# Kernel optimization log

Measured on AMD Instinct MI355X. Metric: run time of the kernel, lower is better.

Reference implementation:

```python
import jax, jax.numpy as jnp
import numpy as np

D_MODEL = 1024
N_HEADS = 16
D_FF = 4096
EPS = 1e-5


def setup_inputs() -> dict:
    key = jax.random.key(0)
    ks = jax.random.split(key, 16)
    s = 0.02
    d, f = D_MODEL, D_FF
    return {
        "x": jax.random.normal(ks[0], (4, 2048, d), dtype=jnp.float32),
        "WQ": jax.random.normal(ks[1], (d, d), dtype=jnp.float32) * s,
        "bQ": jnp.zeros((d,), dtype=jnp.float32),
        "WK": jax.random.normal(ks[2], (d, d), dtype=jnp.float32) * s,
        "bK": jnp.zeros((d,), dtype=jnp.float32),
        "WV": jax.random.normal(ks[3], (d, d), dtype=jnp.float32) * s,
        "bV": jnp.zeros((d,), dtype=jnp.float32),
        "WO": jax.random.normal(ks[4], (d, d), dtype=jnp.float32) * s,
        "bO": jnp.zeros((d,), dtype=jnp.float32),
        "W1": jax.random.normal(ks[5], (f, d), dtype=jnp.float32) * s,
        "b1": jnp.zeros((f,), dtype=jnp.float32),
        "W2": jax.random.normal(ks[6], (d, f), dtype=jnp.float32) * s,
        "b2": jnp.zeros((d,), dtype=jnp.float32),
        "g1": jnp.ones((d,), dtype=jnp.float32),
        "be1": jnp.zeros((d,), dtype=jnp.float32),
        "g2": jnp.ones((d,), dtype=jnp.float32),
        "be2": jnp.zeros((d,), dtype=jnp.float32),
    }


def _layernorm(x, g, b):
    mu = jnp.mean(x, axis=-1, keepdims=True)
    var = jnp.mean(jnp.square(x - mu), axis=-1, keepdims=True)
    return (x - mu) * jax.lax.rsqrt(var + EPS) * g + b


def reference(x, WQ, bQ, WK, bK, WV, bV, WO, bO, W1, b1, W2, b2, g1, be1, g2, be2):
    B, T, D = x.shape
    H, dk = N_HEADS, D // N_HEADS
    # projections (torch Linear: x @ W.T + b), reshape to [B,H,T,dk]
    q = (x @ WQ.T + bQ).reshape(B, T, H, dk).transpose(0, 2, 1, 3)
    k = (x @ WK.T + bK).reshape(B, T, H, dk).transpose(0, 2, 1, 3)
    v = (x @ WV.T + bV).reshape(B, T, H, dk).transpose(0, 2, 1, 3)
    scores = jnp.einsum("bhqd,bhkd->bhqk", q, k) / jnp.sqrt(jnp.float32(dk))
    causal = jnp.tril(jnp.ones((T, T), dtype=bool))
    scores = jnp.where(causal[None, None], scores, jnp.float32(-jnp.inf))
    attn = jax.nn.softmax(scores, axis=-1)
    out = jnp.einsum("bhqk,bhkd->bhqd", attn, v)
    out = out.transpose(0, 2, 1, 3).reshape(B, T, D)
    attn_out = out @ WO.T + bO
    x = _layernorm(x + attn_out, g1, be1)
    ff = jax.nn.relu(x @ W1.T + b1) @ W2.T + b2
    return _layernorm(x + ff, g2, be2)
```

## Files before the change

### kernel.cpp

```cpp
#include <hip/hip_runtime.h>

typedef unsigned short u16;
typedef unsigned int u32;
typedef __bf16 bf16x8 __attribute__((ext_vector_type(8)));
typedef float f32x4 __attribute__((ext_vector_type(4)));

union U16x8 { uint4 u4; u16 us[8]; };

__device__ __forceinline__ u16 f2bf(float f) {
  u32 u = __builtin_bit_cast(u32, f);
  u = (u + 0x7fffu + ((u >> 16) & 1u)) >> 16;
  return (u16)u;
}
__device__ __forceinline__ float bf2f(u16 h) {
  return __builtin_bit_cast(float, ((u32)h) << 16);
}

__device__ __forceinline__ void gll16(const u16* g, u16* l) {
  __builtin_amdgcn_global_load_lds((const __attribute__((address_space(1))) void*)g,
                                   (__attribute__((address_space(3))) void*)l, 16, 0, 0);
}

__global__ __launch_bounds__(256) void cvt_all(const float* __restrict__ x,
                                               const float* __restrict__ WQ,
                                               const float* __restrict__ WK,
                                               const float* __restrict__ WV,
                                               const float* __restrict__ WO,
                                               const float* __restrict__ W1,
                                               const float* __restrict__ W2,
                                               u16* __restrict__ xb,
                                               u16* __restrict__ wqkvb,
                                               u16* __restrict__ wob,
                                               u16* __restrict__ w1b,
                                               u16* __restrict__ w2b) {
  const int S = 1 << 20;
  int i = (blockIdx.x * 256 + threadIdx.x) * 4;
  const float* src;
  u16* dst;
  if (i < 8 * S) { src = x + i; dst = xb + i; }
  else {
    int j = i - 8 * S;
    if (j < 3 * S)      { src = (j < S) ? WQ + j : (j < 2 * S) ? WK + (j - S) : WV + (j - 2 * S);
                          dst = wqkvb + j; }
    else if (j < 4 * S) { src = WO + (j - 3 * S); dst = wob + (j - 3 * S); }
    else if (j < 8 * S) { src = W1 + (j - 4 * S); dst = w1b + (j - 4 * S); }
    else                { src = W2 + (j - 8 * S); dst = w2b + (j - 8 * S); }
  }
  float4 v = *(const float4*)src;
  uint2 o;
  o.x = (u32)f2bf(v.x) | ((u32)f2bf(v.y) << 16);
  o.y = (u32)f2bf(v.z) | ((u32)f2bf(v.w) << 16);
  *(uint2*)dst = o;
}

template <int RELU, int OUT_BF16, int QKV, int SPLIT, int NBN>
__global__ __launch_bounds__(256) void gemm_bt(const u16* __restrict__ A,
                                               const u16* __restrict__ W,
                                               const float* __restrict__ bias0,
                                               void* __restrict__ C0,
                                               int M, int N, int K,
                                               const float* __restrict__ bias1,
                                               void* __restrict__ C1,
                                               const float* __restrict__ bias2,
                                               void* __restrict__ C2) {
  constexpr int NBNC = (NBN > 0) ? NBN : 1;
  __shared__ alignas(16) u16 sA[128 * 64];
  __shared__ alignas(16) u16 sB[128 * 64];
  const int tid = threadIdx.x;
  int bn, bm, koff = 0, KL = K, kz = 0;
  if (SPLIT) {
    const int id = blockIdx.x;
    const int within = id >> 3;
    const int G = (id & 7) + 8 * (within >> 3);
    bn = (within & 7) * 128;
    bm = (G & 63) * 128;
    kz = G >> 6;
    KL = K >> 1;
    koff = kz * KL;
  } else if (NBN > 0) {
    const int id = blockIdx.x;
    const int xcd = id & 7;
    const int r = id >> 3;
    bn = (r % NBNC) * 128;
    bm = ((r / NBNC) * 8 + xcd) * 128;
  } else {
    bn = blockIdx.x * 128;
    bm = blockIdx.y * 128;
  }
  const int lane = tid & 63, wave = tid >> 6;
  const int wm = (wave >> 1) * 64, wn = (wave & 1) * 64;
  const int lr = lane & 15, quad = lane >> 4;
  f32x4 acc[4][4] = {};

  const int srow8 = lane >> 3;
  const int sc = ((lane & 7) ^ srow8) * 8;
  const u16* Ap = A + (size_t)(bm + wave * 32 + srow8) * K + koff + sc;
  const u16* Wp = W + (size_t)(bn + wave * 32 + srow8) * K + koff + sc;
  u16* sAb = sA + wave * 32 * 64;
  u16* sBb = sB + wave * 32 * 64;
  const size_t rK8 = (size_t)8 * K;
  const int fsw = lr & 7;

  for (int kt = 0; kt < KL; kt += 64) {
    __syncthreads();
    #pragma unroll
    for (int j = 0; j < 4; j++) {
      gll16(Ap + kt + j * rK8, sAb + j * 8 * 64);
      gll16(Wp + kt + j * rK8, sBb + j * 8 * 64);
    }
    __syncthreads();
    #pragma unroll
    for (int sl = 0; sl < 2; sl++) {
      bf16x8 af[4], bfr[4];
      #pragma unroll
      for (int mi = 0; mi < 4; mi++)
        af[mi] = *(const bf16x8*)(sA + (wm + mi * 16 + lr) * 64 + ((((sl << 2) | quad) ^ fsw) * 8));
      #pragma unroll
      for (int ni = 0; ni < 4; ni++)
        bfr[ni] = *(const bf16x8*)(sB + (wn + ni * 16 + lr) * 64 + ((((sl << 2) | quad) ^ fsw) * 8));
      #pragma unroll
      for (int mi = 0; mi < 4; mi++)
        #pragma unroll
        for (int ni = 0; ni < 4; ni++)
          acc[mi][ni] = __builtin_amdgcn_mfma_f32_16x16x32_bf16(af[mi], bfr[ni], acc[mi][ni], 0, 0, 0);
    }
  }

  const float* bp = bias0;
  void* outp = C0;
  float scale = 1.0f;
  int cb = bn, Nout = N;
  int seg = 0;
  if (QKV) {
    Nout = 1024;
    seg = bn >> 10;
    cb = bn - (seg << 10);
    if (seg == 0) scale = 0.125f * 1.44269504089f;
    else if (seg == 1) { bp = bias1; outp = C1; }
    else { bp = bias2; outp = C2; }
  }
  if (SPLIT && kz) outp = C1;

  if (QKV && seg == 2) {
    #pragma unroll
    for (int ni = 0; ni < 4; ni++) {
      const int col = cb + wn + ni * 16 + lr;
      const int hh = col >> 6, dl = col & 63;
      const float bv = bp[col];
      #pragma unroll
      for (int mi = 0; mi < 4; mi++) {
        const int row0 = bm + wm + mi * 16 + quad * 4;
        const int bb = row0 >> 11, tt = row0 & 2047;
        u16 pk[4];
        #pragma unroll
        for (int rg = 0; rg < 4; rg++) pk[rg] = f2bf(acc[mi][ni][rg] + bv);
        uint2 val;
        val.x = (u32)pk[0] | ((u32)pk[1] << 16);
        val.y = (u32)pk[2] | ((u32)pk[3] << 16);
        *(uint2*)(((u16*)outp) + ((size_t)((bb * 16 + hh) * 64 + dl)) * 2048 + tt) = val;
      }
    }
    return;
  }

  #pragma unroll
  for (int ni = 0; ni < 4; ni++) {
    const int col = cb + wn + ni * 16 + lr;
    const float bv = (SPLIT && kz) ? 0.0f : bp[col];
    #pragma unroll
    for (int mi = 0; mi < 4; mi++) {
      #pragma unroll
      for (int rg = 0; rg < 4; rg++) {
        int row = bm + wm + mi * 16 + quad * 4 + rg;
        float v = (acc[mi][ni][rg] + bv) * scale;
        if (RELU) v = fmaxf(v, 0.0f);
        if (OUT_BF16) ((u16*)outp)[(size_t)row * Nout + col] = f2bf(v);
        else          ((float*)outp)[(size_t)row * Nout + col] = v;
      }
    }
  }
}

constexpr int ALD = 72;

__global__ __launch_bounds__(256) void attn_mfma(const u16* __restrict__ qb,
                                                 const u16* __restrict__ kb,
                                                 const u16* __restrict__ vt,
                                                 u16* __restrict__ ctxb, int T) {
  __shared__ alignas(16) u16 sK[64 * 64];
  __shared__ alignas(16) u16 sVt[64 * 64];
  __shared__ alignas(16) u16 sP[4 * 2 * 16 * ALD];
  const int tid = threadIdx.x;
  const int i = blockIdx.x;
  const int g = (i & 7) | (((i >> 7) & 7) << 3);
  const int p = (i >> 3) & 15;
  const int h = g >> 2, b = g & 3;
  const size_t base = ((size_t)(b * T)) * 1024 + h * 64;
  const size_t vbase = ((size_t)((b * 16 + h) * 64)) * T;
  const int lane = tid & 63, wave = tid >> 6;
  const int lr = lane & 15, quad = lane >> 4;
  u16* sPA = sP + (wave * 2) * 16 * ALD;
  u16* sPB = sPA + 16 * ALD;

  const int srow = lane >> 3;
  const int sch = ((lane & 7) ^ srow) * 8;
  const int fsw = lr & 7;

  const int qtA = 31 - p, qtB = p;
  const int q0A = qtA * 64 + wave * 16, q0B = qtB * 64 + wave * 16;
  bf16x8 qfA[2], qfB[2];
  #pragma unroll
  for (int sl = 0; sl < 2; sl++) {
    uint4 uA = *(const uint4*)(qb + base + (size_t)(q0A + lr) * 1024 + sl * 32 + quad * 8);
    qfA[sl] = __builtin_bit_cast(bf16x8, uA);
    uint4 uB = *(const uint4*)(qb + base + (size_t)(q0B + lr) * 1024 + sl * 32 + quad * 8);
    qfB[sl] = __builtin_bit_cast(bf16x8, uB);
  }
  f32x4 oA[4] = {}, oB[4] = {};
  float smA[4] = {0, 0, 0, 0}, smB[4] = {0, 0, 0, 0};

  for (int kt = 0; kt <= qtA; kt++) {
    const bool doB = (kt <= qtB);
    __syncthreads();
    #pragma unroll
    for (int j = 0; j < 2; j++) {
      const int rowbase = (wave * 2 + j) * 8;
      const int r = rowbase + srow;
      gll16(kb + base + (size_t)(kt * 64 + r) * 1024 + sch, sK + rowbase * 64);
      gll16(vt + vbase + (size_t)r * T + (size_t)(kt * 64) + sch, sVt + rowbase * 64);
    }
    __syncthreads();

    f32x4 sa[4] = {}, sb[4] = {};
    #pragma unroll
    for (int sl = 0; sl < 2; sl++) {
      bf16x8 kf[4];
      #pragma unroll
      for (int nt = 0; nt < 4; nt++)
        kf[nt] = *(const bf16x8*)(sK + (nt * 16 + lr) * 64 + ((((sl << 2) | quad) ^ fsw) * 8));
      #pragma unroll
      for (int nt = 0; nt < 4; nt++)
        sa[nt] = __builtin_amdgcn_mfma_f32_16x16x32_bf16(kf[nt], qfA[sl], sa[nt], 0, 0, 0);
      if (doB) {
        #pragma unroll
        for (int nt = 0; nt < 4; nt++)
          sb[nt] = __builtin_amdgcn_mfma_f32_16x16x32_bf16(kf[nt], qfB[sl], sb[nt], 0, 0, 0);
      }
    }

    const int qloc = wave * 16 + lr;
    if (kt == qtA) {
      #pragma unroll
      for (int nt = 0; nt < 4; nt++)
        #pragma unroll
        for (int rg = 0; rg < 4; rg++)
          if (nt * 16 + quad * 4 + rg > qloc) sa[nt][rg] = -1e30f;
    }
    if (doB && kt == qtB) {
      #pragma unroll
      for (int nt = 0; nt < 4; nt++)
        #pragma unroll
        for (int rg = 0; rg < 4; rg++)
          if (nt * 16 + quad * 4 + rg > qloc) sb[nt][rg] = -1e30f;
    }

    #pragma unroll
    for (int nt = 0; nt < 4; nt++) {
      float e0 = __builtin_amdgcn_exp2f(sa[nt][0]);
      float e1 = __builtin_amdgcn_exp2f(sa[nt][1]);
      float e2 = __builtin_amdgcn_exp2f(sa[nt][2]);
      float e3 = __builtin_amdgcn_exp2f(sa[nt][3]);
      smA[nt] += (e0 + e1) + (e2 + e3);
      uint2 pk;
      pk.x = __builtin_amdgcn_perm(__builtin_bit_cast(u32, e1), __builtin_bit_cast(u32, e0), 0x07060302u);
      pk.y = __builtin_amdgcn_perm(__builtin_bit_cast(u32, e3), __builtin_bit_cast(u32, e2), 0x07060302u);
      *(uint2*)(sPA + lr * ALD + nt * 16 + quad * 4) = pk;
    }
    if (doB) {
      #pragma unroll
      for (int nt = 0; nt < 4; nt++) {
        float e0 = __builtin_amdgcn_exp2f(sb[nt][0]);
        float e1 = __builtin_amdgcn_exp2f(sb[nt][1]);
        float e2 = __builtin_amdgcn_exp2f(sb[nt][2]);
        float e3 = __builtin_amdgcn_exp2f(sb[nt][3]);
        smB[nt] += (e0 + e1) + (e2 + e3);
        uint2 pk;
        pk.x = __builtin_amdgcn_perm(__builtin_bit_cast(u32, e1), __builtin_bit_cast(u32, e0), 0x07060302u);
        pk.y = __builtin_amdgcn_perm(__builtin_bit_cast(u32, e3), __builtin_bit_cast(u32, e2), 0x07060302u);
        *(uint2*)(sPB + lr * ALD + nt * 16 + quad * 4) = pk;
      }
    }
    asm volatile("" ::: "memory");

    #pragma unroll
    for (int sl = 0; sl < 2; sl++) {
      bf16x8 vf[4];
      #pragma unroll
      for (int nt = 0; nt < 4; nt++)
        vf[nt] = *(const bf16x8*)(sVt + (nt * 16 + lr) * 64 + ((((sl << 2) | quad) ^ fsw) * 8));
      bf16x8 pfA = *(const bf16x8*)(sPA + lr * ALD + sl * 32 + quad * 8);
      #pragma unroll
      for (int nt = 0; nt < 4; nt++)
        oA[nt] = __builtin_amdgcn_mfma_f32_16x16x32_bf16(pfA, vf[nt], oA[nt], 0, 0, 0);
      if (doB) {
        bf16x8 pfB = *(const bf16x8*)(sPB + lr * ALD + sl * 32 + quad * 8);
        #pragma unroll
        for (int nt = 0; nt < 4; nt++)
          oB[nt] = __builtin_amdgcn_mfma_f32_16x16x32_bf16(pfB, vf[nt], oB[nt], 0, 0, 0);
      }
    }
  }

  float sumA = (smA[0] + smA[1]) + (smA[2] + smA[3]);
  sumA += __shfl_xor(sumA, 16);
  sumA += __shfl_xor(sumA, 32);
  float sumB = (smB[0] + smB[1]) + (smB[2] + smB[3]);
  sumB += __shfl_xor(sumB, 16);
  sumB += __shfl_xor(sumB, 32);
  float invA[4], invB[4];
  #pragma unroll
  for (int rg = 0; rg < 4; rg++) {
    invA[rg] = 1.0f / __shfl(sumA, quad * 4 + rg);
    invB[rg] = 1.0f / __shfl(sumB, quad * 4 + rg);
  }
  #pragma unroll
  for (int nt = 0; nt < 4; nt++)
    #pragma unroll
    for (int rg = 0; rg < 4; rg++) {
      int qrow = q0A + quad * 4 + rg;
      ctxb[base + (size_t)qrow * 1024 + nt * 16 + lr] = f2bf(oA[nt][rg] * invA[rg]);
    }
  #pragma unroll
  for (int nt = 0; nt < 4; nt++)
    #pragma unroll
    for (int rg = 0; rg < 4; rg++) {
      int qrow = q0B + quad * 4 + rg;
      ctxb[base + (size_t)qrow * 1024 + nt * 16 + lr] = f2bf(oB[nt][rg] * invB[rg]);
    }
}

template <int ABF>
__global__ __launch_bounds__(256) void ln_kernel(const void* __restrict__ a,
                                                 const u16* __restrict__ b,
                                                 const u16* __restrict__ c,
                                                 const float* __restrict__ g,
                                                 const float* __restrict__ be,
                                                 float* __restrict__ of32,
                                                 u16* __restrict__ obf) {
  const int row = blockIdx.x;
  const int tid = threadIdx.x;
  const size_t base = (size_t)row * 1024;
  const int cc = tid * 4;
  float a0, a1, a2, a3;
  if (ABF) {
    uint2 ua = *(const uint2*)((const u16*)a + base + cc);
    a0 = bf2f(ua.x & 0xffff); a1 = bf2f(ua.x >> 16);
    a2 = bf2f(ua.y & 0xffff); a3 = bf2f(ua.y >> 16);
  } else {
    float4 xa = *(const float4*)((const float*)a + base + cc);
    a0 = xa.x; a1 = xa.y; a2 = xa.z; a3 = xa.w;
  }
  uint2 ub = *(const uint2*)(b + base + cc);
  uint2 uc = *(const uint2*)(c + base + cc);
  float v0 = a0 + bf2f(ub.x & 0xffff) + bf2f(uc.x & 0xffff);
  float v1 = a1 + bf2f(ub.x >> 16)    + bf2f(uc.x >> 16);
  float v2 = a2 + bf2f(ub.y & 0xffff) + bf2f(uc.y & 0xffff);
  float v3 = a3 + bf2f(ub.y >> 16)    + bf2f(uc.y >> 16);
  float s1 = v0 + v1 + v2 + v3;
  float s2 = v0 * v0 + v1 * v1 + v2 * v2 + v3 * v3;
  for (int off = 1; off < 64; off <<= 1) {
    s1 += __shfl_xor(s1, off);
    s2 += __shfl_xor(s2, off);
  }
  __shared__ float red[8];
  int wv = tid >> 6;
  if ((tid & 63) == 0) { red[wv] = s1; red[4 + wv] = s2; }
  __syncthreads();
  s1 = red[0] + red[1] + red[2] + red[3];
  s2 = red[4] + red[5] + red[6] + red[7];
  float mu = s1 * (1.0f / 1024.0f);
  float var = s2 * (1.0f / 1024.0f) - mu * mu;
  float rs = rsqrtf(var + 1e-5f);
  float4 gv = *(const float4*)(g + cc);
  float4 bev = *(const float4*)(be + cc);
  float y0 = (v0 - mu) * rs * gv.x + bev.x;
  float y1 = (v1 - mu) * rs * gv.y + bev.y;
  float y2 = (v2 - mu) * rs * gv.z + bev.z;
  float y3 = (v3 - mu) * rs * gv.w + bev.w;
  if (of32) {
    float4 o = make_float4(y0, y1, y2, y3);
    *(float4*)(of32 + base + cc) = o;
  }
  if (obf) {
    uint2 o;
    o.x = (u32)f2bf(y0) | ((u32)f2bf(y1) << 16);
    o.y = (u32)f2bf(y2) | ((u32)f2bf(y3) << 16);
    *(uint2*)(obf + base + cc) = o;
  }
}

extern "C" void kernel_launch(void* const* d_in, const int* in_sizes, int n_in,
                              void* d_out, int out_size, void* d_ws, size_t ws_size,
                              hipStream_t stream) {
  const int Mtok = 8192, D = 1024, F = 4096, T = 2048;
  const float* x   = (const float*)d_in[0];
  const float* WQ  = (const float*)d_in[1];
  const float* bQ  = (const float*)d_in[2];
  const float* WK  = (const float*)d_in[3];
  const float* bK  = (const float*)d_in[4];
  const float* WV  = (const float*)d_in[5];
  const float* bV  = (const float*)d_in[6];
  const float* WO  = (const float*)d_in[7];
  const float* bO  = (const float*)d_in[8];
  const float* W1  = (const float*)d_in[9];
  const float* b1  = (const float*)d_in[10];
  const float* W2  = (const float*)d_in[11];
  const float* b2  = (const float*)d_in[12];
  const float* g1  = (const float*)d_in[13];
  const float* be1 = (const float*)d_in[14];
  const float* g2  = (const float*)d_in[15];
  const float* be2 = (const float*)d_in[16];

  char* ws = (char*)d_ws;
  const size_t MB = 1024 * 1024;
  u16*  xb     = (u16*)(ws + 0);
  u16*  wqkvb  = (u16*)(ws + 16 * MB);
  u16*  wob    = (u16*)(ws + 22 * MB);
  u16*  w1b    = (u16*)(ws + 24 * MB);
  u16*  w2b    = (u16*)(ws + 32 * MB);
  u16*  qb     = (u16*)(ws + 40 * MB);
  u16*  kb     = (u16*)(ws + 56 * MB);
  u16*  vtb    = (u16*)(ws + 72 * MB);
  u16*  ctxb   = (u16*)(ws + 88 * MB);
  u16*  wp0    = (u16*)(ws + 104 * MB);
  u16*  wp1    = (u16*)(ws + 120 * MB);
  u16*  h1b    = (u16*)(ws + 136 * MB);
  u16*  ff1b   = (u16*)(ws + 40 * MB);
  u16*  fp0    = (u16*)(ws + 0);
  u16*  fp1    = (u16*)(ws + 16 * MB);
  float* out   = (float*)d_out;

  dim3 blk(256);
  cvt_all<<<(20 << 20) / 1024, blk, 0, stream>>>(x, WQ, WK, WV, WO, W1, W2,
                                                 xb, wqkvb, wob, w1b, w2b);

  gemm_bt<0, 1, 1, 0, 24><<<dim3(1536), blk, 0, stream>>>(xb, wqkvb, bQ, qb, Mtok, 3072, D,
                                                          bK, kb, bV, vtb);
  attn_mfma<<<dim3(1024), blk, 0, stream>>>(qb, kb, vtb, ctxb, T);

  gemm_bt<0, 1, 0, 1, 0><<<dim3(1024), blk, 0, stream>>>(ctxb, wob, bO, wp0, Mtok, D, D,
                                                         nullptr, wp1, nullptr, nullptr);
  ln_kernel<0><<<Mtok, blk, 0, stream>>>(x, wp0, wp1, g1, be1, nullptr, h1b);

  gemm_bt<1, 1, 0, 0, 32><<<dim3(2048), blk, 0, stream>>>(h1b, w1b, b1, ff1b, Mtok, F, D,
                                                          nullptr, nullptr, nullptr, nullptr);
  gemm_bt<0, 1, 0, 1, 0><<<dim3(1024), blk, 0, stream>>>(ff1b, w2b, b2, fp0, Mtok, D, F,
                                                         nullptr, fp1, nullptr, nullptr);
  ln_kernel<1><<<Mtok, blk, 0, stream>>>(h1b, fp0, fp1, g2, be2, out, (u16*)nullptr);
}
```

Measured before the change: 528.4 us.

## Replace 128x128 GEMM with 256x256 tile, 512-thread, 4-stage pipelined kernel

Replaces the 128x128-tile, 256-thread GEMM (load, sync, compute) with a 256x256-tile, 8-wave kernel. It uses a 4-deep LDS ring buffer of BK=32 slices with direct global-to-LDS loads issued three tiles ahead, explicit vmcnt/lgkmcnt waits and raw barriers. MFMA bursts are raised with setprio, and loads are interleaved between the two half-tile compute phases. The larger tile is meant to raise arithmetic intensity and hide memory latency, but it needs 128 KB of LDS and large accumulators, which limits occupancy and leaves fewer blocks per GEMM.

New measurement: 505.1 us. 4.4% less time.

```diff
diff --git a/kernel.cpp b/kernel.cpp
--- a/kernel.cpp
+++ b/kernel.cpp
@@ -5,8 +5,6 @@
 typedef __bf16 bf16x8 __attribute__((ext_vector_type(8)));
 typedef float f32x4 __attribute__((ext_vector_type(4)));
 
-union U16x8 { uint4 u4; u16 us[8]; };
-
 __device__ __forceinline__ u16 f2bf(float f) {
   u32 u = __builtin_bit_cast(u32, f);
   u = (u + 0x7fffu + ((u >> 16) & 1u)) >> 16;
@@ -20,6 +18,15 @@
   __builtin_amdgcn_global_load_lds((const __attribute__((address_space(1))) void*)g,
                                    (__attribute__((address_space(3))) void*)l, 16, 0, 0);
 }
+
+__device__ __forceinline__ void barrier() {
+  asm volatile("" ::: "memory");
+  __builtin_amdgcn_s_barrier();
+  asm volatile("" ::: "memory");
+}
+__device__ __forceinline__ void waitv8() { asm volatile("s_waitcnt vmcnt(8)" ::: "memory"); }
+__device__ __forceinline__ void waitv0() { asm volatile("s_waitcnt vmcnt(0)" ::: "memory"); }
+__device__ __forceinline__ void waitlgk0() { asm volatile("s_waitcnt lgkmcnt(0)" ::: "memory"); }
 
 __global__ __launch_bounds__(256) void cvt_all(const float* __restrict__ x,
                                                const float* __restrict__ WQ,
@@ -53,88 +60,114 @@
   *(uint2*)dst = o;
 }
 
-template <int RELU, int OUT_BF16, int QKV, int SPLIT, int NBN>
-__global__ __launch_bounds__(256) void gemm_bt(const u16* __restrict__ A,
-                                               const u16* __restrict__ W,
-                                               const float* __restrict__ bias0,
-                                               void* __restrict__ C0,
-                                               int M, int N, int K,
-                                               const float* __restrict__ bias1,
-                                               void* __restrict__ C1,
-                                               const float* __restrict__ bias2,
-                                               void* __restrict__ C2) {
-  constexpr int NBNC = (NBN > 0) ? NBN : 1;
-  __shared__ alignas(16) u16 sA[128 * 64];
-  __shared__ alignas(16) u16 sB[128 * 64];
+template <int RELU, int QKV, int SPLIT>
+__global__ __launch_bounds__(512, 2) void gemm256(const u16* __restrict__ A,
+                                                  const u16* __restrict__ W,
+                                                  const float* __restrict__ bias0,
+                                                  void* __restrict__ C0,
+                                                  int M, int N, int K,
+                                                  const float* __restrict__ bias1,
+                                                  void* __restrict__ C1,
+                                                  const float* __restrict__ bias2,
+                                                  void* __restrict__ C2,
+                                                  int NBN) {
+  __shared__ alignas(16) u16 lds[4 * 16384];
   const int tid = threadIdx.x;
-  int bn, bm, koff = 0, KL = K, kz = 0;
+  const int id = blockIdx.x;
+  const int xcd = id & 7, r = id >> 3;
+  int bm, bn, kz = 0, koff = 0, KL = K;
   if (SPLIT) {
-    const int id = blockIdx.x;
-    const int within = id >> 3;
-    const int G = (id & 7) + 8 * (within >> 3);
-    bn = (within & 7) * 128;
-    bm = (G & 63) * 128;
-    kz = G >> 6;
+    bn = (r & 3) << 8;
+    const int q = r >> 2;
+    bm = ((q & 3) * 8 + xcd) << 8;
+    kz = q >> 2;
     KL = K >> 1;
     koff = kz * KL;
-  } else if (NBN > 0) {
-    const int id = blockIdx.x;
-    const int xcd = id & 7;
-    const int r = id >> 3;
-    bn = (r % NBNC) * 128;
-    bm = ((r / NBNC) * 8 + xcd) * 128;
   } else {
-    bn = blockIdx.x * 128;
-    bm = blockIdx.y * 128;
-  }
-  const int lane = tid & 63, wave = tid >> 6;
-  const int wm = (wave >> 1) * 64, wn = (wave & 1) * 64;
+    bn = (r % NBN) << 8;
+    bm = ((r / NBN) * 8 + xcd) << 8;
+  }
+  const int wave = tid >> 6, lane = tid & 63;
   const int lr = lane & 15, quad = lane >> 4;
-  f32x4 acc[4][4] = {};
-
-  const int srow8 = lane >> 3;
-  const int sc = ((lane & 7) ^ srow8) * 8;
-  const u16* Ap = A + (size_t)(bm + wave * 32 + srow8) * K + koff + sc;
-  const u16* Wp = W + (size_t)(bn + wave * 32 + srow8) * K + koff + sc;
-  u16* sAb = sA + wave * 32 * 64;
-  u16* sBb = sB + wave * 32 * 64;
-  const size_t rK8 = (size_t)8 * K;
-  const int fsw = lr & 7;
-
-  for (int kt = 0; kt < KL; kt += 64) {
-    __syncthreads();
-    #pragma unroll
-    for (int j = 0; j < 4; j++) {
-      gll16(Ap + kt + j * rK8, sAb + j * 8 * 64);
-      gll16(Wp + kt + j * rK8, sBb + j * 8 * 64);
-    }
-    __syncthreads();
-    #pragma unroll
-    for (int sl = 0; sl < 2; sl++) {
-      bf16x8 af[4], bfr[4];
-      #pragma unroll
-      for (int mi = 0; mi < 4; mi++)
-        af[mi] = *(const bf16x8*)(sA + (wm + mi * 16 + lr) * 64 + ((((sl << 2) | quad) ^ fsw) * 8));
+  const int wm = (wave >> 2) << 7;
+  const int wn = (wave & 3) << 6;
+
+  const int lrow = lane >> 2;
+  const int lch = (lane & 3) ^ ((lane >> 3) & 3);
+  const u16* Asrc = A + (size_t)(bm + wave * 16 + lrow) * K + koff + lch * 8;
+  const u16* Wsrc = W + (size_t)(bn + wave * 16 + lrow) * K + koff + lch * 8;
+  const size_t half = (size_t)128 * K;
+  u16* dstbase = lds + wave * 512;
+
+  const int NT = KL >> 5;
+  const int fro = (quad ^ ((lr >> 1) & 3)) * 8;
+  f32x4 acc[8][4] = {};
+
+  #pragma unroll
+  for (int t = 0; t < 3; t++) {
+    u16* d = dstbase + t * 16384;
+    gll16(Asrc + (size_t)t * 32, d);
+    gll16(Asrc + (size_t)t * 32 + half, d + 4096);
+    gll16(Wsrc + (size_t)t * 32, d + 8192);
+    gll16(Wsrc + (size_t)t * 32 + half, d + 12288);
+  }
+  waitv8();
+  barrier();
+
+  for (int t = 0; t < NT; t++) {
+    const u16* sa = lds + (t & 3) * 16384;
+    const u16* sb = sa + 8192;
+    const int tp = (t + 3 < NT) ? t + 3 : NT - 1;
+    u16* d = dstbase + ((t + 3) & 3) * 16384;
+    const size_t ko = (size_t)tp * 32;
+
+    bf16x8 af[4], bfr[4];
+    #pragma unroll
+    for (int mi = 0; mi < 4; mi++)
+      af[mi] = *(const bf16x8*)(sa + (wm + mi * 16 + lr) * 32 + fro);
+    #pragma unroll
+    for (int ni = 0; ni < 4; ni++)
+      bfr[ni] = *(const bf16x8*)(sb + (wn + ni * 16 + lr) * 32 + fro);
+    gll16(Asrc + ko, d);
+    gll16(Asrc + ko + half, d + 4096);
+    barrier();
+    waitlgk0();
+    __builtin_amdgcn_s_setprio(1);
+    #pragma unroll
+    for (int mi = 0; mi < 4; mi++)
       #pragma unroll
       for (int ni = 0; ni < 4; ni++)
-        bfr[ni] = *(const bf16x8*)(sB + (wn + ni * 16 + lr) * 64 + ((((sl << 2) | quad) ^ fsw) * 8));
-      #pragma unroll
-      for (int mi = 0; mi < 4; mi++)
-        #pragma unroll
-        for (int ni = 0; ni < 4; ni++)
-          acc[mi][ni] = __builtin_amdgcn_mfma_f32_16x16x32_bf16(af[mi], bfr[ni], acc[mi][ni], 0, 0, 0);
-    }
-  }
+        acc[mi][ni] = __builtin_amdgcn_mfma_f32_16x16x32_bf16(af[mi], bfr[ni], acc[mi][ni], 0, 0, 0);
+    __builtin_amdgcn_s_setprio(0);
+    barrier();
+
+    #pragma unroll
+    for (int mi = 0; mi < 4; mi++)
+      af[mi] = *(const bf16x8*)(sa + (wm + 64 + mi * 16 + lr) * 32 + fro);
+    gll16(Wsrc + ko, d + 8192);
+    gll16(Wsrc + ko + half, d + 12288);
+    barrier();
+    waitlgk0();
+    __builtin_amdgcn_s_setprio(1);
+    #pragma unroll
+    for (int mi = 0; mi < 4; mi++)
+      #pragma unroll
+      for (int ni = 0; ni < 4; ni++)
+        acc[4 + mi][ni] = __builtin_amdgcn_mfma_f32_16x16x32_bf16(af[mi], bfr[ni], acc[4 + mi][ni], 0, 0, 0);
+    __builtin_amdgcn_s_setprio(0);
+    waitv8();
+    barrier();
+  }
+  waitv0();
 
   const float* bp = bias0;
   void* outp = C0;
   float scale = 1.0f;
-  int cb = bn, Nout = N;
-  int seg = 0;
+  int cb = bn, Nout = N, seg = 0;
   if (QKV) {
     Nout = 1024;
     seg = bn >> 10;
-    cb = bn - (seg << 10);
+    cb = bn & 1023;
     if (seg == 0) scale = 0.125f * 1.44269504089f;
     else if (seg == 1) { bp = bias1; outp = C1; }
     else { bp = bias2; outp = C2; }
@@ -148,7 +181,7 @@
       const int hh = col >> 6, dl = col & 63;
       const float bv = bp[col];
       #pragma unroll
-      for (int mi = 0; mi < 4; mi++) {
+      for (int mi = 0; mi < 8; mi++) {
         const int row0 = bm + wm + mi * 16 + quad * 4;
         const int bb = row0 >> 11, tt = row0 & 2047;
         u16 pk[4];
@@ -168,14 +201,13 @@
     const int col = cb + wn + ni * 16 + lr;
     const float bv = (SPLIT && kz) ? 0.0f : bp[col];
     #pragma unroll
-    for (int mi = 0; mi < 4; mi++) {
+    for (int mi = 0; mi < 8; mi++) {
       #pragma unroll
       for (int rg = 0; rg < 4; rg++) {
         int row = bm + wm + mi * 16 + quad * 4 + rg;
         float v = (acc[mi][ni][rg] + bv) * scale;
         if (RELU) v = fmaxf(v, 0.0f);
-        if (OUT_BF16) ((u16*)outp)[(size_t)row * Nout + col] = f2bf(v);
-        else          ((float*)outp)[(size_t)row * Nout + col] = v;
+        ((u16*)outp)[(size_t)row * Nout + col] = f2bf(v);
       }
     }
   }
@@ -441,20 +473,21 @@
   float* out   = (float*)d_out;
 
   dim3 blk(256);
+  dim3 blk512(512);
   cvt_all<<<(20 << 20) / 1024, blk, 0, stream>>>(x, WQ, WK, WV, WO, W1, W2,
                                                  xb, wqkvb, wob, w1b, w2b);
 
-  gemm_bt<0, 1, 1, 0, 24><<<dim3(1536), blk, 0, stream>>>(xb, wqkvb, bQ, qb, Mtok, 3072, D,
-                                                          bK, kb, bV, vtb);
+  gemm256<0, 1, 0><<<dim3(384), blk512, 0, stream>>>(xb, wqkvb, bQ, qb, Mtok, 3072, D,
+                                                     bK, kb, bV, vtb, 12);
   attn_mfma<<<dim3(1024), blk, 0, stream>>>(qb, kb, vtb, ctxb, T);
 
-  gemm_bt<0, 1, 0, 1, 0><<<dim3(1024), blk, 0, stream>>>(ctxb, wob, bO, wp0, Mtok, D, D,
-                                                         nullptr, wp1, nullptr, nullptr);
+  gemm256<0, 0, 1><<<dim3(256), blk512, 0, stream>>>(ctxb, wob, bO, wp0, Mtok, D, D,
+                                                     nullptr, wp1, nullptr, nullptr, 4);
   ln_kernel<0><<<Mtok, blk, 0, stream>>>(x, wp0, wp1, g1, be1, nullptr, h1b);
 
-  gemm_bt<1, 1, 0, 0, 32><<<dim3(2048), blk, 0, stream>>>(h1b, w1b, b1, ff1b, Mtok, F, D,
-                                                          nullptr, nullptr, nullptr, nullptr);
-  gemm_bt<0, 1, 0, 1, 0><<<dim3(1024), blk, 0, stream>>>(ff1b, w2b, b2, fp0, Mtok, D, F,
-                                                         nullptr, fp1, nullptr, nullptr);
+  gemm256<1, 0, 0><<<dim3(512), blk512, 0, stream>>>(h1b, w1b, b1, ff1b, Mtok, F, D,
+                                                     nullptr, nullptr, nullptr, nullptr, 16);
+  gemm256<0, 0, 1><<<dim3(256), blk512, 0, stream>>>(ff1b, w2b, b2, fp0, Mtok, D, F,
+                                                     nullptr, fp1, nullptr, nullptr, 4);
   ln_kernel<1><<<Mtok, blk, 0, stream>>>(h1b, fp0, fp1, g2, be2, out, (u16*)nullptr);
 }
```
